# Optimization experiments

Measured on AMD Instinct MI355X. Metric: run time of the kernel, lower is better.

Reference implementation:

```python
import jax, jax.numpy as jnp
import numpy as np

N_NODES = 50000
N_HEDGES = 10000
NNZ_INC = 400000
NNZ_E = 80000
NNZ_V = 400000
VDIM = 128
EDIM = 128
OUT_VDIM = 128
OUT_EDIM = 128


def _spmm(rows, cols, vals, X, n_rows):
    # sparse COO [n_rows, n_cols] @ X  -> [n_rows, d]
    return jax.ops.segment_sum(vals[:, None] * X[cols], rows, num_segments=n_rows)


def setup_inputs() -> dict:
    key = jax.random.key(0)
    ks = jax.random.split(key, 20)
    inp = {
        "vfeat": jax.random.normal(ks[0], (N_NODES, VDIM), jnp.float32),
        "efeat": jax.random.normal(ks[1], (N_HEDGES, EDIM), jnp.float32),
        "invDV": jax.random.uniform(ks[2], (N_NODES,), jnp.float32),
        "invDE": jax.random.uniform(ks[3], (N_HEDGES,), jnp.float32),
        "inc_src": jax.random.randint(ks[4], (NNZ_INC,), 0, N_NODES, jnp.int32),
        "inc_dst": jax.random.randint(ks[5], (NNZ_INC,), 0, N_HEDGES, jnp.int32),
        "emat_rows": jax.random.randint(ks[6], (NNZ_E,), 0, N_HEDGES, jnp.int32),
        "emat_cols": jax.random.randint(ks[7], (NNZ_E,), 0, N_HEDGES, jnp.int32),
        "emat_vals": jax.random.normal(ks[8], (NNZ_E,), jnp.float32),
        "vmat_rows": jax.random.randint(ks[9], (NNZ_V,), 0, N_NODES, jnp.int32),
        "vmat_cols": jax.random.randint(ks[10], (NNZ_V,), 0, N_NODES, jnp.int32),
        "vmat_vals": jax.random.normal(ks[11], (NNZ_V,), jnp.float32),
        # parameters (torch Linear: y = x @ W.T + b)
        "Wv": jax.random.normal(ks[12], (OUT_VDIM, VDIM), jnp.float32) * 0.05,
        "We": jax.random.normal(ks[13], (OUT_EDIM, EDIM), jnp.float32) * 0.05,
        "psi1_W": jax.random.normal(ks[14], (VDIM, VDIM + EDIM), jnp.float32) * 0.05,
        "psi1_b": jnp.zeros((VDIM,), jnp.float32),
        "psi2_W": jax.random.normal(ks[15], (EDIM, OUT_VDIM + EDIM), jnp.float32) * 0.05,
        "psi2_b": jnp.zeros((EDIM,), jnp.float32),
    }
    return inp


def reference(vfeat, efeat, invDV, invDE, inc_src, inc_dst,
              emat_rows, emat_cols, emat_vals,
              vmat_rows, vmat_cols, vmat_vals,
              Wv, We, psi1_W, psi1_b, psi2_W, psi2_b):
    N = vfeat.shape[0]
    E = efeat.shape[0]
    # --- 'in' update_all with psi1: per-incidence concat -> linear -> *invDV[src] -> sum into hyperedge
    x = jnp.concatenate([vfeat[inc_src], efeat[inc_dst]], axis=1)  # [nnz, VDIM+EDIM]
    x = x @ psi1_W.T + psi1_b                                       # [nnz, VDIM]
    x = x * invDV[inc_src][:, None]
    A = jax.ops.segment_sum(x, inc_dst, num_segments=E)             # [E, VDIM]
    A = _spmm(emat_rows, emat_cols, emat_vals, A, E)
    _efeat = A + efeat
    # --- 'con' update_all: node gathers sum of incident hyperedge feats
    _vfeat = jax.ops.segment_sum(_efeat[inc_dst], inc_src, num_segments=N)
    vfeat_out = jax.nn.relu(_vfeat @ Wv.T)                           # [N, OUT_VDIM]
    # --- 'in' update_all with psi2 (dv = ones)
    x2 = jnp.concatenate([vfeat_out[inc_src], efeat[inc_dst]], axis=1)
    x2 = x2 @ psi2_W.T + psi2_b                                      # [nnz, EDIM]
    B = jax.ops.segment_sum(x2, inc_dst, num_segments=E) * invDE[:, None]
    # --- 'con' pass with efeat, then vMat spmm, then 'in' sum back to hyperedges
    _vfeat2 = jax.ops.segment_sum(efeat[inc_dst], inc_src, num_segments=N)
    _vfeat2 = _spmm(vmat_rows, vmat_cols, vmat_vals, _vfeat2, N)
    _efeat2 = jax.ops.segment_sum(_vfeat2[inc_src], inc_dst, num_segments=E)
    _efeat2 = _efeat2 + B
    efeat_out = jax.nn.relu(_efeat2 @ We.T)                          # [E, OUT_EDIM]
    return vfeat_out, efeat_out
```

## Files before the change

kernel.cpp:

```cpp
#include <hip/hip_runtime.h>

#define NN 50000
#define NE 10000
#define NNZ_INC 400000
#define NNZ_E 80000
#define NNZ_V 400000
#define D 128
#define KC 32

#define CAP_D 112
#define CAP_S 40
#define CAP_E 40
#define CAP_V 40

#define NE_SH (NE / 8)
#define NN_SH (NN / 8)

#define GN_ 782
#define GE_ 157
#define G_HINC ((NNZ_INC + 255) / 256)
#define G_HIST8 (8 * G_HINC)
#define G_EV ((NNZ_E + NNZ_V + 255) / 256)
#define G_CVTN 6250
#define G_CVTE 1250
#define G_NR16 (NN / 16)
#define G_ER16 (NE / 16)

typedef unsigned short u16;
typedef unsigned int u32;

__device__ __forceinline__ u16 f2bf(float x) {
    unsigned u = __float_as_uint(x);
    unsigned r = u + 0x7fffu + ((u >> 16) & 1u);
    return (u16)(r >> 16);
}
__device__ __forceinline__ float bf2f(u16 h) {
    return __uint_as_float(((unsigned)h) << 16);
}

__device__ __forceinline__ void acc8(uint4 u, float acc[8]) {
    acc[0] += __uint_as_float(u.x << 16);
    acc[1] += __uint_as_float(u.x & 0xffff0000u);
    acc[2] += __uint_as_float(u.y << 16);
    acc[3] += __uint_as_float(u.y & 0xffff0000u);
    acc[4] += __uint_as_float(u.z << 16);
    acc[5] += __uint_as_float(u.z & 0xffff0000u);
    acc[6] += __uint_as_float(u.w << 16);
    acc[7] += __uint_as_float(u.w & 0xffff0000u);
}
__device__ __forceinline__ void fma8(uint4 u, float v, float acc[8]) {
    acc[0] = fmaf(v, __uint_as_float(u.x << 16), acc[0]);
    acc[1] = fmaf(v, __uint_as_float(u.x & 0xffff0000u), acc[1]);
    acc[2] = fmaf(v, __uint_as_float(u.y << 16), acc[2]);
    acc[3] = fmaf(v, __uint_as_float(u.y & 0xffff0000u), acc[3]);
    acc[4] = fmaf(v, __uint_as_float(u.z << 16), acc[4]);
    acc[5] = fmaf(v, __uint_as_float(u.z & 0xffff0000u), acc[5]);
    acc[6] = fmaf(v, __uint_as_float(u.w << 16), acc[6]);
    acc[7] = fmaf(v, __uint_as_float(u.w & 0xffff0000u), acc[7]);
}
__device__ __forceinline__ uint4 pack_bf8(const float acc[8]) {
    uint4 o;
    o.x = (u32)f2bf(acc[0]) | ((u32)f2bf(acc[1]) << 16);
    o.y = (u32)f2bf(acc[2]) | ((u32)f2bf(acc[3]) << 16);
    o.z = (u32)f2bf(acc[4]) | ((u32)f2bf(acc[5]) << 16);
    o.w = (u32)f2bf(acc[6]) | ((u32)f2bf(acc[7]) << 16);
    return o;
}

__device__ __forceinline__ void gemm_acc(
    int bx, const float* __restrict__ X, const float* __restrict__ W, int ldw,
    int M, float acc[8][4])
{
    __shared__ float XsT[KC][68];
    __shared__ float Ws[KC][132];
    const int tid = threadIdx.x;
    const int tx = tid & 31, ty = tid >> 5;
    const int row0 = bx * 64;
    const int c0 = tx * 4;
    const int r0 = ty * 8;

#pragma unroll
    for (int r = 0; r < 8; ++r)
#pragma unroll
        for (int c = 0; c < 4; ++c) acc[r][c] = 0.f;

    for (int kc = 0; kc < D; kc += KC) {
        __syncthreads();
#pragma unroll
        for (int it = 0; it < 2; ++it) {
            int l = tid + it * 256;
            int r = l >> 3, k4 = l & 7;
            float4 v = make_float4(0.f, 0.f, 0.f, 0.f);
            int row = row0 + r;
            if (row < M) v = ((const float4*)(X + (size_t)row * D + kc))[k4];
            int k = k4 * 4;
            XsT[k + 0][r] = v.x; XsT[k + 1][r] = v.y;
            XsT[k + 2][r] = v.z; XsT[k + 3][r] = v.w;
        }
#pragma unroll
        for (int it = 0; it < 4; ++it) {
            int l = tid + it * 256;
            int o = l >> 3, k4 = l & 7;
            float4 w = ((const float4*)(W + (size_t)o * ldw + kc))[k4];
            int k = k4 * 4;
            Ws[k + 0][o] = w.x; Ws[k + 1][o] = w.y;
            Ws[k + 2][o] = w.z; Ws[k + 3][o] = w.w;
        }
        __syncthreads();
#pragma unroll
        for (int k = 0; k < KC; ++k) {
            const float4 a0 = *(const float4*)&XsT[k][r0];
            const float4 a1 = *(const float4*)&XsT[k][r0 + 4];
            const float4 b  = *(const float4*)&Ws[k][c0];
            float av[8] = {a0.x, a0.y, a0.z, a0.w, a1.x, a1.y, a1.z, a1.w};
            float bv[4] = {b.x, b.y, b.z, b.w};
#pragma unroll
            for (int r = 0; r < 8; ++r)
#pragma unroll
                for (int c = 0; c < 4; ++c)
                    acc[r][c] = fmaf(av[r], bv[c], acc[r][c]);
        }
    }
}

__device__ __forceinline__ void gemm_acc2(
    int bx, const float* __restrict__ X1, const float* __restrict__ X2,
    const float* __restrict__ rsf,
    const float* __restrict__ W, int M, float acc[8][4])
{
    __shared__ float XsT[KC][68];
    __shared__ float Ws[KC][132];
    const int tid = threadIdx.x;
    const int tx = tid & 31, ty = tid >> 5;
    const int row0 = bx * 64;
    const int c0 = tx * 4;
    const int r0 = ty * 8;

#pragma unroll
    for (int r = 0; r < 8; ++r)
#pragma unroll
        for (int c = 0; c < 4; ++c) acc[r][c] = 0.f;

    for (int kc = 0; kc < 2 * D; kc += KC) {
        __syncthreads();
        const bool second = (kc >= D);
        const float* Xp = second ? X2 : X1;
        const int kk = second ? kc - D : kc;
#pragma unroll
        for (int it = 0; it < 2; ++it) {
            int l = tid + it * 256;
            int r = l >> 3, k4 = l & 7;
            float4 v = make_float4(0.f, 0.f, 0.f, 0.f);
            int row = row0 + r;
            if (row < M) {
                v = ((const float4*)(Xp + (size_t)row * D + kk))[k4];
                if (second) {
                    float sc = rsf[row];
                    v.x *= sc; v.y *= sc; v.z *= sc; v.w *= sc;
                }
            }
            int k = k4 * 4;
            XsT[k + 0][r] = v.x; XsT[k + 1][r] = v.y;
            XsT[k + 2][r] = v.z; XsT[k + 3][r] = v.w;
        }
#pragma unroll
        for (int it = 0; it < 4; ++it) {
            int l = tid + it * 256;
            int o = l >> 3, k4 = l & 7;
            float4 w = ((const float4*)(W + (size_t)o * (2 * D) + kc))[k4];
            int k = k4 * 4;
            Ws[k + 0][o] = w.x; Ws[k + 1][o] = w.y;
            Ws[k + 2][o] = w.z; Ws[k + 3][o] = w.w;
        }
        __syncthreads();
#pragma unroll
        for (int k = 0; k < KC; ++k) {
            const float4 a0 = *(const float4*)&XsT[k][r0];
            const float4 a1 = *(const float4*)&XsT[k][r0 + 4];
            const float4 b  = *(const float4*)&Ws[k][c0];
            float av[8] = {a0.x, a0.y, a0.z, a0.w, a1.x, a1.y, a1.z, a1.w};
            float bv[4] = {b.x, b.y, b.z, b.w};
#pragma unroll
            for (int r = 0; r < 8; ++r)
#pragma unroll
                for (int c = 0; c < 4; ++c)
                    acc[r][c] = fmaf(av[r], bv[c], acc[r][c]);
        }
    }
}

__global__ __launch_bounds__(256) void mega0(
    const int* __restrict__ inc_src, const int* __restrict__ inc_dst,
    int* __restrict__ cnt_dst, int* __restrict__ cnt_src,
    u16* __restrict__ ell_d, u16* __restrict__ ell_s,
    const float* __restrict__ efeat, const float* __restrict__ vfeat,
    const float* __restrict__ invDV,
    u16* __restrict__ vfi_b, u16* __restrict__ efeat_b)
{
    int b = blockIdx.x;
    if (b < G_HIST8) {
        int shard = b & 7;
        int i = (b >> 3) * 256 + threadIdx.x;
        if (i < NNZ_INC) {
            int s = inc_src[i], d = inc_dst[i];
            if ((u32)(d - shard * NE_SH) < (u32)NE_SH) {
                int rd = atomicAdd(cnt_dst + d, 1);
                if (rd < CAP_D) ell_d[d * CAP_D + rd] = (u16)s;
            }
            if ((u32)(s - shard * NN_SH) < (u32)NN_SH) {
                int rs = atomicAdd(cnt_src + s, 1);
                if (rs < CAP_S) ell_s[s * CAP_S + rs] = (u16)d;
            }
        }
    } else if (b < G_HIST8 + G_CVTN) {
        int i = ((b - G_HIST8) * 256 + threadIdx.x) * 4;
        int row = i >> 7;
        float s = invDV[row];
        float4 v = *(const float4*)(vfeat + i);
        ushort4 u;
        u.x = f2bf(v.x * s); u.y = f2bf(v.y * s);
        u.z = f2bf(v.z * s); u.w = f2bf(v.w * s);
        *(ushort4*)(vfi_b + i) = u;
    } else {
        int i = ((b - G_HIST8 - G_CVTN) * 256 + threadIdx.x) * 4;
        float4 v = *(const float4*)(efeat + i);
        ushort4 u;
        u.x = f2bf(v.x); u.y = f2bf(v.y); u.z = f2bf(v.z); u.w = f2bf(v.w);
        *(ushort4*)(efeat_b + i) = u;
    }
}

__device__ __forceinline__ void segsum_bf_ell16(int rb,
    const int* __restrict__ cnt, int cap, const u16* __restrict__ ell,
    const u16* __restrict__ Tb, u16* __restrict__ Yb, int R)
{
    int r = rb * 16 + (threadIdx.x >> 4);
    int q = threadIdx.x & 15;
    if (r >= R) return;
    int m = min(cnt[r], cap);
    const u16* lst = ell + (size_t)r * cap;
    float acc[8] = {0.f, 0.f, 0.f, 0.f, 0.f, 0.f, 0.f, 0.f};
    int j = 0;
    for (; j + 3 < m; j += 4) {
        ushort4 ix = *(const ushort4*)(lst + j);
        uint4 u0 = *(const uint4*)(Tb + (size_t)ix.x * D + q * 8);
        uint4 u1 = *(const uint4*)(Tb + (size_t)ix.y * D + q * 8);
        uint4 u2 = *(const uint4*)(Tb + (size_t)ix.z * D + q * 8);
        uint4 u3 = *(const uint4*)(Tb + (size_t)ix.w * D + q * 8);
        acc8(u0, acc); acc8(u1, acc); acc8(u2, acc); acc8(u3, acc);
    }
    for (; j < m; ++j) {
        uint4 u0 = *(const uint4*)(Tb + (size_t)lst[j] * D + q * 8);
        acc8(u0, acc);
    }
    ((uint4*)(Yb + (size_t)r * D))[q] = pack_bf8(acc);
}

__device__ __forceinline__ void segsum_f_ell16(int rb,
    const int* __restrict__ cnt, int cap, const u16* __restrict__ ell,
    const u16* __restrict__ Tb, float* __restrict__ Y, int R)
{
    int r = rb * 16 + (threadIdx.x >> 4);
    int q = threadIdx.x & 15;
    if (r >= R) return;
    int m = min(cnt[r], cap);
    const u16* lst = ell + (size_t)r * cap;
    float acc[8] = {0.f, 0.f, 0.f, 0.f, 0.f, 0.f, 0.f, 0.f};
    int j = 0;
    for (; j + 7 < m; j += 8) {
        ushort4 ixa = *(const ushort4*)(lst + j);
        ushort4 ixb = *(const ushort4*)(lst + j + 4);
        uint4 u0 = *(const uint4*)(Tb + (size_t)ixa.x * D + q * 8);
        uint4 u1 = *(const uint4*)(Tb + (size_t)ixa.y * D + q * 8);
        uint4 u2 = *(const uint4*)(Tb + (size_t)ixa.z * D + q * 8);
        uint4 u3 = *(const uint4*)(Tb + (size_t)ixa.w * D + q * 8);
        uint4 u4 = *(const uint4*)(Tb + (size_t)ixb.x * D + q * 8);
        uint4 u5 = *(const uint4*)(Tb + (size_t)ixb.y * D + q * 8);
        uint4 u6 = *(const uint4*)(Tb + (size_t)ixb.z * D + q * 8);
        uint4 u7 = *(const uint4*)(Tb + (size_t)ixb.w * D + q * 8);
        acc8(u0, acc); acc8(u1, acc); acc8(u2, acc); acc8(u3, acc);
        acc8(u4, acc); acc8(u5, acc); acc8(u6, acc); acc8(u7, acc);
    }
    for (; j + 3 < m; j += 4) {
        ushort4 ix = *(const ushort4*)(lst + j);
        uint4 u0 = *(const uint4*)(Tb + (size_t)ix.x * D + q * 8);
        uint4 u1 = *(const uint4*)(Tb + (size_t)ix.y * D + q * 8);
        uint4 u2 = *(const uint4*)(Tb + (size_t)ix.z * D + q * 8);
        uint4 u3 = *(const uint4*)(Tb + (size_t)ix.w * D + q * 8);
        acc8(u0, acc); acc8(u1, acc); acc8(u2, acc); acc8(u3, acc);
    }
    for (; j < m; ++j) {
        uint4 u0 = *(const uint4*)(Tb + (size_t)lst[j] * D + q * 8);
        acc8(u0, acc);
    }
    float* yr = Y + (size_t)r * D;
    ((float4*)yr)[2 * q + 0] = make_float4(acc[0], acc[1], acc[2], acc[3]);
    ((float4*)yr)[2 * q + 1] = make_float4(acc[4], acc[5], acc[6], acc[7]);
}

__device__ __forceinline__ void spmm_bf_ell16(int rb,
    const int* __restrict__ cnt, int cap, const u32* __restrict__ ell,
    const u16* __restrict__ Xb, const float* __restrict__ addend,
    u16* __restrict__ Yb, int R)
{
    int r = rb * 16 + (threadIdx.x >> 4);
    int q = threadIdx.x & 15;
    if (r >= R) return;
    int m = min(cnt[r], cap);
    const u32* lst = ell + (size_t)r * cap;
    float acc[8];
    if (addend) {
        const float* ar = addend + (size_t)r * D;
        float4 lo = ((const float4*)ar)[2 * q + 0];
        float4 hi = ((const float4*)ar)[2 * q + 1];
        acc[0] = lo.x; acc[1] = lo.y; acc[2] = lo.z; acc[3] = lo.w;
        acc[4] = hi.x; acc[5] = hi.y; acc[6] = hi.z; acc[7] = hi.w;
    } else {
#pragma unroll
        for (int i = 0; i < 8; ++i) acc[i] = 0.f;
    }
    int j = 0;
    for (; j + 3 < m; j += 4) {
        uint4 e = *(const uint4*)(lst + j);
        uint4 x0 = *(const uint4*)(Xb + (size_t)(e.x >> 16) * D + q * 8);
        uint4 x1 = *(const uint4*)(Xb + (size_t)(e.y >> 16) * D + q * 8);
        uint4 x2 = *(const uint4*)(Xb + (size_t)(e.z >> 16) * D + q * 8);
        uint4 x3 = *(const uint4*)(Xb + (size_t)(e.w >> 16) * D + q * 8);
        fma8(x0, __uint_as_float(e.x << 16), acc);
        fma8(x1, __uint_as_float(e.y << 16), acc);
        fma8(x2, __uint_as_float(e.z << 16), acc);
        fma8(x3, __uint_as_float(e.w << 16), acc);
    }
    for (; j < m; ++j) {
        u32 e = lst[j];
        uint4 x = *(const uint4*)(Xb + (size_t)(e >> 16) * D + q * 8);
        fma8(x, __uint_as_float(e << 16), acc);
    }
    ((uint4*)(Yb + (size_t)r * D))[q] = pack_bf8(acc);
}

__global__ __launch_bounds__(256) void fusedA(
    const int* __restrict__ erows, const int* __restrict__ ecols,
    const float* __restrict__ evals, int* __restrict__ cnt_e, u32* __restrict__ ev_e,
    const int* __restrict__ vrows, const int* __restrict__ vcols,
    const float* __restrict__ vvals, int* __restrict__ cnt_v, u32* __restrict__ ev_v,
    const float* __restrict__ efeat,
    const float* __restrict__ psi2_W, const float* __restrict__ psi2_b, float* __restrict__ QeP,
    const int* __restrict__ cnt_dst, const u16* __restrict__ ell_d,
    const float* __restrict__ invDV, const u16* __restrict__ vfi_b,
    float* __restrict__ sva, float* __restrict__ wsum,
    const int* __restrict__ cnt_src, const u16* __restrict__ ell_s,
    const u16* __restrict__ efeat_b, u16* __restrict__ vf2_b)
{
    int b = blockIdx.x;
    if (b < G_EV) {
        int i = b * 256 + threadIdx.x;
        if (i < NNZ_E) {
            int r = erows[i];
            int re = atomicAdd(cnt_e + r, 1);
            if (re < CAP_E)
                ev_e[r * CAP_E + re] = ((u32)ecols[i] << 16) | (u32)f2bf(evals[i]);
        } else if (i < NNZ_E + NNZ_V) {
            int j = i - NNZ_E;
            int r = vrows[j];
            int rv = atomicAdd(cnt_v + r, 1);
            if (rv < CAP_V)
                ev_v[r * CAP_V + rv] = ((u32)vcols[j] << 16) | (u32)f2bf(vvals[j]);
        }
    } else if (b < G_EV + GE_) {
        int bx = b - G_EV;
        float acc[8][4];
        gemm_acc(bx, efeat, psi2_W + D, 2 * D, NE, acc);
        int tx = threadIdx.x & 31, ty = threadIdx.x >> 5;
        float4 b4 = ((const float4*)psi2_b)[tx];
#pragma unroll
        for (int r = 0; r < 8; ++r) {
            int row = bx * 64 + ty * 8 + r;
            if (row < NE) {
                float4 v = make_float4(acc[r][0] + b4.x, acc[r][1] + b4.y,
                                       acc[r][2] + b4.z, acc[r][3] + b4.w);
                ((float4*)(QeP + (size_t)row * D))[tx] = v;
            }
        }
    } else if (b < G_EV + GE_ + G_ER16) {
        int e = (b - G_EV - GE_) * 16 + (threadIdx.x >> 4);
        int q = threadIdx.x & 15;
        if (e >= NE) return;
        int m = min(cnt_dst[e], CAP_D);
        const u16* lst = ell_d + (size_t)e * CAP_D;
        float acc[8] = {0.f, 0.f, 0.f, 0.f, 0.f, 0.f, 0.f, 0.f};
        float ws = 0.f;
        int j = 0;
        for (; j + 3 < m; j += 4) {
            ushort4 ix = *(const ushort4*)(lst + j);
            uint4 u0 = *(const uint4*)(vfi_b + (size_t)ix.x * D + q * 8);
            uint4 u1 = *(const uint4*)(vfi_b + (size_t)ix.y * D + q * 8);
            uint4 u2 = *(const uint4*)(vfi_b + (size_t)ix.z * D + q * 8);
            uint4 u3 = *(const uint4*)(vfi_b + (size_t)ix.w * D + q * 8);
            ws += (invDV[ix.x] + invDV[ix.y]) + (invDV[ix.z] + invDV[ix.w]);
            acc8(u0, acc); acc8(u1, acc); acc8(u2, acc); acc8(u3, acc);
        }
        for (; j < m; ++j) {
            int s = lst[j];
            uint4 u0 = *(const uint4*)(vfi_b + (size_t)s * D + q * 8);
            ws += invDV[s];
            acc8(u0, acc);
        }
        float* yr = sva + (size_t)e * D;
        ((float4*)yr)[2 * q + 0] = make_float4(acc[0], acc[1], acc[2], acc[3]);
        ((float4*)yr)[2 * q + 1] = make_float4(acc[4], acc[5], acc[6], acc[7]);
        if (q == 0) wsum[e] = ws;
    } else {
        segsum_bf_ell16(b - G_EV - GE_ - G_ER16, cnt_src, CAP_S, ell_s, efeat_b, vf2_b, NN);
    }
}

__global__ __launch_bounds__(256) void fusedB2(
    const float* __restrict__ sva, const float* __restrict__ efeat,
    const float* __restrict__ wsum,
    const float* __restrict__ psi1_W, const float* __restrict__ psi1_b,
    u16* __restrict__ A_b,
    const int* __restrict__ cnt_v, const u32* __restrict__ ev_v,
    const u16* __restrict__ vf2_b, u16* __restrict__ vf2b_b)
{
    int b = blockIdx.x;
    if (b < GE_) {
        float acc[8][4];
        gemm_acc2(b, sva, efeat, wsum, psi1_W, NE, acc);
        int tx = threadIdx.x & 31, ty = threadIdx.x >> 5;
        float4 b4 = ((const float4*)psi1_b)[tx];
#pragma unroll
        for (int r = 0; r < 8; ++r) {
            int row = b * 64 + ty * 8 + r;
            if (row < NE) {
                float ws = wsum[row];
                ushort4 u;
                u.x = f2bf(fmaf(ws, b4.x, acc[r][0]));
                u.y = f2bf(fmaf(ws, b4.y, acc[r][1]));
                u.z = f2bf(fmaf(ws, b4.z, acc[r][2]));
                u.w = f2bf(fmaf(ws, b4.w, acc[r][3]));
                ((ushort4*)(A_b + (size_t)row * D))[tx] = u;
            }
        }
    } else {
        spmm_bf_ell16(b - GE_, cnt_v, CAP_V, ev_v, vf2_b, nullptr, vf2b_b, NN);
    }
}

__global__ __launch_bounds__(256) void fusedC2(
    const int* __restrict__ cnt_e, const u32* __restrict__ ev_e,
    const u16* __restrict__ A_b, const float* __restrict__ efeat, u16* __restrict__ A2_b,
    const int* __restrict__ cnt_dst, const u16* __restrict__ ell_d,
    const u16* __restrict__ vf2b_b, float* __restrict__ av)
{
    int b = blockIdx.x;
    if (b < G_ER16) spmm_bf_ell16(b, cnt_e, CAP_E, ev_e, A_b, efeat, A2_b, NE);
    else segsum_f_ell16(b - G_ER16, cnt_dst, CAP_D, ell_d, vf2b_b, av, NE);
}

__global__ __launch_bounds__(256) void fusedD2(
    const int* __restrict__ cnt_src, const u16* __restrict__ ell_s,
    const u16* __restrict__ A2_b, float* __restrict__ vf1)
{
    segsum_f_ell16(blockIdx.x, cnt_src, CAP_S, ell_s, A2_b, vf1, NN);
}

__global__ __launch_bounds__(256) void gemmC_k(
    const float* __restrict__ vf1, const float* __restrict__ Wv,
    float* __restrict__ out_v, u16* __restrict__ outv_b)
{
    float acc[8][4];
    gemm_acc(blockIdx.x, vf1, Wv, D, NN, acc);
    int tx = threadIdx.x & 31, ty = threadIdx.x >> 5;
#pragma unroll
    for (int r = 0; r < 8; ++r) {
        int row = blockIdx.x * 64 + ty * 8 + r;
        if (row < NN) {
            float4 v = make_float4(fmaxf(acc[r][0], 0.f), fmaxf(acc[r][1], 0.f),
                                   fmaxf(acc[r][2], 0.f), fmaxf(acc[r][3], 0.f));
            ((float4*)(out_v + (size_t)row * D))[tx] = v;
            ushort4 u;
            u.x = f2bf(v.x); u.y = f2bf(v.y); u.z = f2bf(v.z); u.w = f2bf(v.w);
            ((ushort4*)(outv_b + (size_t)row * D))[tx] = u;
        }
    }
}

__global__ __launch_bounds__(256) void gather_sv(
    const int* __restrict__ cnt_dst, const u16* __restrict__ ell_d,
    const u16* __restrict__ outv_b, float* __restrict__ sv)
{
    segsum_f_ell16(blockIdx.x, cnt_dst, CAP_D, ell_d, outv_b, sv, NE);
}

__global__ __launch_bounds__(256) void gemmBE_k(
    const float* __restrict__ sv, const float* __restrict__ psi2_W,
    const int* __restrict__ cnt_dst, const float* __restrict__ QeP,
    const float* __restrict__ invDE, const float* __restrict__ av,
    const float* __restrict__ We, float* __restrict__ out_e)
{
    __shared__ float T[D][68];
    float acc[8][4];
    gemm_acc(blockIdx.x, sv, psi2_W, 2 * D, NE, acc);
    const int tx = threadIdx.x & 31, ty = threadIdx.x >> 5;
    const int bx = blockIdx.x;
#pragma unroll
    for (int r = 0; r < 8; ++r) {
        int row = bx * 64 + ty * 8 + r;
        float deg = 0.f, ide = 0.f;
        float4 qe = make_float4(0.f, 0.f, 0.f, 0.f);
        float4 a  = make_float4(0.f, 0.f, 0.f, 0.f);
        if (row < NE) {
            deg = (float)cnt_dst[row];
            ide = invDE[row];
            qe = ((const float4*)(QeP + (size_t)row * D))[tx];
            a  = ((const float4*)(av  + (size_t)row * D))[tx];
        }
        int lr = ty * 8 + r;
        T[tx * 4 + 0][lr] = fmaf(deg, qe.x, acc[r][0]) * ide + a.x;
        T[tx * 4 + 1][lr] = fmaf(deg, qe.y, acc[r][1]) * ide + a.y;
        T[tx * 4 + 2][lr] = fmaf(deg, qe.z, acc[r][2]) * ide + a.z;
        T[tx * 4 + 3][lr] = fmaf(deg, qe.w, acc[r][3]) * ide + a.w;
    }
    __shared__ float Ws2[KC][132];
    float acc2[8][4];
#pragma unroll
    for (int r = 0; r < 8; ++r)
#pragma unroll
        for (int c = 0; c < 4; ++c) acc2[r][c] = 0.f;
    const int c0 = tx * 4, r0 = ty * 8;
    for (int kc = 0; kc < D; kc += KC) {
        __syncthreads();
#pragma unroll
        for (int it = 0; it < 4; ++it) {
            int l = threadIdx.x + it * 256;
            int o = l >> 3, k4 = l & 7;
            float4 w = ((const float4*)(We + (size_t)o * D + kc))[k4];
            int k = k4 * 4;
            Ws2[k + 0][o] = w.x; Ws2[k + 1][o] = w.y;
            Ws2[k + 2][o] = w.z; Ws2[k + 3][o] = w.w;
        }
        __syncthreads();
#pragma unroll
        for (int k = 0; k < KC; ++k) {
            const float4 a0 = *(const float4*)&T[kc + k][r0];
            const float4 a1 = *(const float4*)&T[kc + k][r0 + 4];
            const float4 bb = *(const float4*)&Ws2[k][c0];
            float avv[8] = {a0.x, a0.y, a0.z, a0.w, a1.x, a1.y, a1.z, a1.w};
            float bv[4] = {bb.x, bb.y, bb.z, bb.w};
#pragma unroll
            for (int r = 0; r < 8; ++r)
#pragma unroll
                for (int c = 0; c < 4; ++c)
                    acc2[r][c] = fmaf(avv[r], bv[c], acc2[r][c]);
        }
    }
#pragma unroll
    for (int r = 0; r < 8; ++r) {
        int row = bx * 64 + ty * 8 + r;
        if (row < NE) {
            float4 v = make_float4(fmaxf(acc2[r][0], 0.f), fmaxf(acc2[r][1], 0.f),
                                   fmaxf(acc2[r][2], 0.f), fmaxf(acc2[r][3], 0.f));
            ((float4*)(out_e + (size_t)row * D))[tx] = v;
        }
    }
}

extern "C" void kernel_launch(void* const* d_in, const int* in_sizes, int n_in,
                              void* d_out, int out_size, void* d_ws, size_t ws_size,
                              hipStream_t stream)
{
    (void)in_sizes; (void)n_in; (void)out_size; (void)ws_size;
    const float* vfeat     = (const float*)d_in[0];
    const float* efeat     = (const float*)d_in[1];
    const float* invDV     = (const float*)d_in[2];
    const float* invDE     = (const float*)d_in[3];
    const int*   inc_src   = (const int*)d_in[4];
    const int*   inc_dst   = (const int*)d_in[5];
    const int*   emat_rows = (const int*)d_in[6];
    const int*   emat_cols = (const int*)d_in[7];
    const float* emat_vals = (const float*)d_in[8];
    const int*   vmat_rows = (const int*)d_in[9];
    const int*   vmat_cols = (const int*)d_in[10];
    const float* vmat_vals = (const float*)d_in[11];
    const float* Wv        = (const float*)d_in[12];
    const float* We        = (const float*)d_in[13];
    const float* psi1_W    = (const float*)d_in[14];
    const float* psi1_b    = (const float*)d_in[15];
    const float* psi2_W    = (const float*)d_in[16];
    const float* psi2_b    = (const float*)d_in[17];

    const size_t ND = (size_t)NN * D;
    const size_t ED = (size_t)NE * D;

    char* p = (char*)d_ws;
    auto alloc = [&](size_t bytes) {
        size_t a = (size_t)p; a = (a + 255) & ~(size_t)255;
        p = (char*)a; void* r = (void*)p; p += bytes; return r;
    };
    float* QeP   = (float*)alloc(ED * 4);
    float* vf1   = (float*)alloc(ND * 4);
    float* av    = (float*)alloc(ED * 4);
    float* svbuf = (float*)alloc(ED * 4);
    float* wsum  = (float*)alloc((size_t)NE * 4);
    u16* vfi_b   = (u16*)alloc(ND * 2);
    u16* outv_b  = (u16*)alloc(ND * 2);
    u16* vf2_b   = (u16*)alloc(ND * 2);
    u16* vf2b_b  = (u16*)alloc(ND * 2);
    u16* efeat_b = (u16*)alloc(ED * 2);
    u16* A_b     = (u16*)alloc(ED * 2);
    u16* A2_b    = (u16*)alloc(ED * 2);
    int* cnt_dst = (int*)alloc((size_t)(2 * NE + 2 * NN) * 4);
    int* cnt_src = cnt_dst + NE;
    int* cnt_e   = cnt_src + NN;
    int* cnt_v   = cnt_e + NE;
    u16* ell_d   = (u16*)alloc((size_t)NE * CAP_D * 2);
    u16* ell_s   = (u16*)alloc((size_t)NN * CAP_S * 2);
    u32* ev_e    = (u32*)alloc((size_t)NE * CAP_E * 4);
    u32* ev_v    = (u32*)alloc((size_t)NN * CAP_V * 4);

    float* out_v = (float*)d_out;
    float* out_e = out_v + ND;

    dim3 b256(256);

    hipMemsetAsync(cnt_dst, 0, (size_t)(2 * NE + 2 * NN) * sizeof(int), stream);
    mega0<<<G_HIST8 + G_CVTN + G_CVTE, b256, 0, stream>>>(
        inc_src, inc_dst, cnt_dst, cnt_src, ell_d, ell_s,
        efeat, vfeat, invDV, vfi_b, efeat_b);
    fusedA<<<G_EV + GE_ + G_ER16 + G_NR16, b256, 0, stream>>>(
        emat_rows, emat_cols, emat_vals, cnt_e, ev_e,
        vmat_rows, vmat_cols, vmat_vals, cnt_v, ev_v,
        efeat, psi2_W, psi2_b, QeP,
        cnt_dst, ell_d, invDV, vfi_b, svbuf, wsum,
        cnt_src, ell_s, efeat_b, vf2_b);
    fusedB2<<<GE_ + G_NR16, b256, 0, stream>>>(
        svbuf, efeat, wsum, psi1_W, psi1_b, A_b,
        cnt_v, ev_v, vf2_b, vf2b_b);
    fusedC2<<<G_ER16 + G_ER16, b256, 0, stream>>>(
        cnt_e, ev_e, A_b, efeat, A2_b,
        cnt_dst, ell_d, vf2b_b, av);
    fusedD2<<<G_NR16, b256, 0, stream>>>(cnt_src, ell_s, A2_b, vf1);
    gemmC_k<<<GN_, b256, 0, stream>>>(vf1, Wv, out_v, outv_b);
    gather_sv<<<G_ER16, b256, 0, stream>>>(cnt_dst, ell_d, outv_b, svbuf);
    gemmBE_k<<<GE_, b256, 0, stream>>>(svbuf, psi2_W, cnt_dst, QeP, invDE, av, We, out_e);
}
```

Before: 362.5 us.

## Apply Wv on hyperedge side before node gather, add ELL sorting, fold COO build into mega0

Uses linearity to move the Wv projection from the 50000-row node GEMM to the 10000-row hyperedge side. It applies Wv to efeat and to the psi1 output, chained inside fusedB2, so the node pass becomes a gather-sum plus ReLU. This removes the separate node GEMM kernel and the fp32 vf1 intermediate. The emat/vmat COO-to-ELL build moves into the first mega kernel. A new insertion-sort kernel orders each ELL row's indices to improve gather locality, at the cost of an extra launch and serial per-thread sorting.

```diff
diff --git a/kernel.cpp b/kernel.cpp
--- a/kernel.cpp
+++ b/kernel.cpp
@@ -16,15 +16,16 @@
 #define NE_SH (NE / 8)
 #define NN_SH (NN / 8)
 
-#define GN_ 782
 #define GE_ 157
 #define G_HINC ((NNZ_INC + 255) / 256)
 #define G_HIST8 (8 * G_HINC)
-#define G_EV ((NNZ_E + NNZ_V + 255) / 256)
+#define G_EVB ((NNZ_E + NNZ_V + 255) / 256)
 #define G_CVTN 6250
 #define G_CVTE 1250
 #define G_NR16 (NN / 16)
 #define G_ER16 (NE / 16)
+#define G_SORT_D 40
+#define G_SORT_V 196
 
 typedef unsigned short u16;
 typedef unsigned int u32;
@@ -123,76 +124,14 @@
     }
 }
 
-__device__ __forceinline__ void gemm_acc2(
-    int bx, const float* __restrict__ X1, const float* __restrict__ X2,
-    const float* __restrict__ rsf,
-    const float* __restrict__ W, int M, float acc[8][4])
-{
-    __shared__ float XsT[KC][68];
-    __shared__ float Ws[KC][132];
-    const int tid = threadIdx.x;
-    const int tx = tid & 31, ty = tid >> 5;
-    const int row0 = bx * 64;
-    const int c0 = tx * 4;
-    const int r0 = ty * 8;
-
-#pragma unroll
-    for (int r = 0; r < 8; ++r)
-#pragma unroll
-        for (int c = 0; c < 4; ++c) acc[r][c] = 0.f;
-
-    for (int kc = 0; kc < 2 * D; kc += KC) {
-        __syncthreads();
-        const bool second = (kc >= D);
-        const float* Xp = second ? X2 : X1;
-        const int kk = second ? kc - D : kc;
-#pragma unroll
-        for (int it = 0; it < 2; ++it) {
-            int l = tid + it * 256;
-            int r = l >> 3, k4 = l & 7;
-            float4 v = make_float4(0.f, 0.f, 0.f, 0.f);
-            int row = row0 + r;
-            if (row < M) {
-                v = ((const float4*)(Xp + (size_t)row * D + kk))[k4];
-                if (second) {
-                    float sc = rsf[row];
-                    v.x *= sc; v.y *= sc; v.z *= sc; v.w *= sc;
-                }
-            }
-            int k = k4 * 4;
-            XsT[k + 0][r] = v.x; XsT[k + 1][r] = v.y;
-            XsT[k + 2][r] = v.z; XsT[k + 3][r] = v.w;
-        }
-#pragma unroll
-        for (int it = 0; it < 4; ++it) {
-            int l = tid + it * 256;
-            int o = l >> 3, k4 = l & 7;
-            float4 w = ((const float4*)(W + (size_t)o * (2 * D) + kc))[k4];
-            int k = k4 * 4;
-            Ws[k + 0][o] = w.x; Ws[k + 1][o] = w.y;
-            Ws[k + 2][o] = w.z; Ws[k + 3][o] = w.w;
-        }
-        __syncthreads();
-#pragma unroll
-        for (int k = 0; k < KC; ++k) {
-            const float4 a0 = *(const float4*)&XsT[k][r0];
-            const float4 a1 = *(const float4*)&XsT[k][r0 + 4];
-            const float4 b  = *(const float4*)&Ws[k][c0];
-            float av[8] = {a0.x, a0.y, a0.z, a0.w, a1.x, a1.y, a1.z, a1.w};
-            float bv[4] = {b.x, b.y, b.z, b.w};
-#pragma unroll
-            for (int r = 0; r < 8; ++r)
-#pragma unroll
-                for (int c = 0; c < 4; ++c)
-                    acc[r][c] = fmaf(av[r], bv[c], acc[r][c]);
-        }
-    }
-}
-
 __global__ __launch_bounds__(256) void mega0(
     const int* __restrict__ inc_src, const int* __restrict__ inc_dst,
     int* __restrict__ cnt_dst, int* __restrict__ cnt_src,
     u16* __restrict__ ell_d, u16* __restrict__ ell_s,
+    const int* __restrict__ erows, const int* __restrict__ ecols,
+    const float* __restrict__ evals, int* __restrict__ cnt_e, u32* __restrict__ ev_e,
+    const int* __restrict__ vrows, const int* __restrict__ vcols,
+    const float* __restrict__ vvals, int* __restrict__ cnt_v, u32* __restrict__ ev_v,
     const float* __restrict__ efeat, const float* __restrict__ vfeat,
     const float* __restrict__ invDV,
     u16* __restrict__ vfi_b, u16* __restrict__ efeat_b)
@@ -212,8 +151,22 @@
                 if (rs < CAP_S) ell_s[s * CAP_S + rs] = (u16)d;
             }
         }
-    } else if (b < G_HIST8 + G_CVTN) {
-        int i = ((b - G_HIST8) * 256 + threadIdx.x) * 4;
+    } else if (b < G_HIST8 + G_EVB) {
+        int i = (b - G_HIST8) * 256 + threadIdx.x;
+        if (i < NNZ_E) {
+            int r = erows[i];
+            int re = atomicAdd(cnt_e + r, 1);
+            if (re < CAP_E)
+                ev_e[r * CAP_E + re] = ((u32)ecols[i] << 16) | (u32)f2bf(evals[i]);
+        } else if (i < NNZ_E + NNZ_V) {
+            int j = i - NNZ_E;
+            int r = vrows[j];
+            int rv = atomicAdd(cnt_v + r, 1);
+            if (rv < CAP_V)
+                ev_v[r * CAP_V + rv] = ((u32)vcols[j] << 16) | (u32)f2bf(vvals[j]);
+        }
+    } else if (b < G_HIST8 + G_EVB + G_CVTN) {
+        int i = ((b - G_HIST8 - G_EVB) * 256 + threadIdx.x) * 4;
         int row = i >> 7;
         float s = invDV[row];
         float4 v = *(const float4*)(vfeat + i);
@@ -222,11 +175,41 @@
         u.z = f2bf(v.z * s); u.w = f2bf(v.w * s);
         *(ushort4*)(vfi_b + i) = u;
     } else {
-        int i = ((b - G_HIST8 - G_CVTN) * 256 + threadIdx.x) * 4;
+        int i = ((b - G_HIST8 - G_EVB - G_CVTN) * 256 + threadIdx.x) * 4;
         float4 v = *(const float4*)(efeat + i);
         ushort4 u;
         u.x = f2bf(v.x); u.y = f2bf(v.y); u.z = f2bf(v.z); u.w = f2bf(v.w);
         *(ushort4*)(efeat_b + i) = u;
+    }
+}
+
+__global__ __launch_bounds__(256) void sortk(
+    const int* __restrict__ cnt_dst, u16* __restrict__ ell_d,
+    const int* __restrict__ cnt_v, u32* __restrict__ ev_v)
+{
+    int b = blockIdx.x;
+    if (b < G_SORT_D) {
+        int r = b * 256 + threadIdx.x;
+        if (r >= NE) return;
+        int m = min(cnt_dst[r], CAP_D);
+        u16* a = ell_d + (size_t)r * CAP_D;
+        for (int i = 1; i < m; ++i) {
+            u16 key = a[i];
+            int j = i - 1;
+            while (j >= 0 && a[j] > key) { a[j + 1] = a[j]; --j; }
+            a[j + 1] = key;
+        }
+    } else {
+        int r = (b - G_SORT_D) * 256 + threadIdx.x;
+        if (r >= NN) return;
+        int m = min(cnt_v[r], CAP_V);
+        u32* a = ev_v + (size_t)r * CAP_V;
+        for (int i = 1; i < m; ++i) {
+            u32 key = a[i];
+            int j = i - 1;
+            while (j >= 0 && a[j] > key) { a[j + 1] = a[j]; --j; }
+            a[j + 1] = key;
+        }
     }
 }
 
@@ -340,12 +323,9 @@
 }
 
 __global__ __launch_bounds__(256) void fusedA(
-    const int* __restrict__ erows, const int* __restrict__ ecols,
-    const float* __restrict__ evals, int* __restrict__ cnt_e, u32* __restrict__ ev_e,
-    const int* __restrict__ vrows, const int* __restrict__ vcols,
-    const float* __restrict__ vvals, int* __restrict__ cnt_v, u32* __restrict__ ev_v,
     const float* __restrict__ efeat,
     const float* __restrict__ psi2_W, const float* __restrict__ psi2_b, float* __restrict__ QeP,
+    const float* __restrict__ Wv, float* __restrict__ efP,
     const int* __restrict__ cnt_dst, const u16* __restrict__ ell_d,
     const float* __restrict__ invDV, const u16* __restrict__ vfi_b,
     float* __restrict__ sva, float* __restrict__ wsum,
@@ -353,37 +333,8 @@
     const u16* __restrict__ efeat_b, u16* __restrict__ vf2_b)
 {
     int b = blockIdx.x;
-    if (b < G_EV) {
-        int i = b * 256 + threadIdx.x;
-        if (i < NNZ_E) {
-            int r = erows[i];
-            int re = atomicAdd(cnt_e + r, 1);
-            if (re < CAP_E)
-                ev_e[r * CAP_E + re] = ((u32)ecols[i] << 16) | (u32)f2bf(evals[i]);
-        } else if (i < NNZ_E + NNZ_V) {
-            int j = i - NNZ_E;
-            int r = vrows[j];
-            int rv = atomicAdd(cnt_v + r, 1);
-            if (rv < CAP_V)
-                ev_v[r * CAP_V + rv] = ((u32)vcols[j] << 16) | (u32)f2bf(vvals[j]);
-        }
-    } else if (b < G_EV + GE_) {
-        int bx = b - G_EV;
-        float acc[8][4];
-        gemm_acc(bx, efeat, psi2_W + D, 2 * D, NE, acc);
-        int tx = threadIdx.x & 31, ty = threadIdx.x >> 5;
-        float4 b4 = ((const float4*)psi2_b)[tx];
-#pragma unroll
-        for (int r = 0; r < 8; ++r) {
-            int row = bx * 64 + ty * 8 + r;
-            if (row < NE) {
-                float4 v = make_float4(acc[r][0] + b4.x, acc[r][1] + b4.y,
-                                       acc[r][2] + b4.z, acc[r][3] + b4.w);
-                ((float4*)(QeP + (size_t)row * D))[tx] = v;
-            }
-        }
-    } else if (b < G_EV + GE_ + G_ER16) {
-        int e = (b - G_EV - GE_) * 16 + (threadIdx.x >> 4);
+    if (b < G_ER16) {
+        int e = b * 16 + (threadIdx.x >> 4);
         int q = threadIdx.x & 15;
         if (e >= NE) return;
         int m = min(cnt_dst[e], CAP_D);
@@ -410,8 +361,36 @@
         ((float4*)yr)[2 * q + 0] = make_float4(acc[0], acc[1], acc[2], acc[3]);
         ((float4*)yr)[2 * q + 1] = make_float4(acc[4], acc[5], acc[6], acc[7]);
         if (q == 0) wsum[e] = ws;
+    } else if (b < G_ER16 + GE_) {
+        int bx = b - G_ER16;
+        float acc[8][4];
+        gemm_acc(bx, efeat, psi2_W + D, 2 * D, NE, acc);
+        int tx = threadIdx.x & 31, ty = threadIdx.x >> 5;
+        float4 b4 = ((const float4*)psi2_b)[tx];
+#pragma unroll
+        for (int r = 0; r < 8; ++r) {
+            int row = bx * 64 + ty * 8 + r;
+            if (row < NE) {
+                float4 v = make_float4(acc[r][0] + b4.x, acc[r][1] + b4.y,
+                                       acc[r][2] + b4.z, acc[r][3] + b4.w);
+                ((float4*)(QeP + (size_t)row * D))[tx] = v;
+            }
+        }
+    } else if (b < G_ER16 + 2 * GE_) {
+        int bx = b - G_ER16 - GE_;
+        float acc[8][4];
+        gemm_acc(bx, efeat, Wv, D, NE, acc);
+        int tx = threadIdx.x & 31, ty = threadIdx.x >> 5;
+#pragma unroll
+        for (int r = 0; r < 8; ++r) {
+            int row = bx * 64 + ty * 8 + r;
+            if (row < NE) {
+                float4 v = make_float4(acc[r][0], acc[r][1], acc[r][2], acc[r][3]);
+                ((float4*)(efP + (size_t)row * D))[tx] = v;
+            }
+        }
     } else {
-        segsum_bf_ell16(b - G_EV - GE_ - G_ER16, cnt_src, CAP_S, ell_s, efeat_b, vf2_b, NN);
+        segsum_bf_ell16(b - G_ER16 - 2 * GE_, cnt_src, CAP_S, ell_s, efeat_b, vf2_b, NN);
     }
 }
 
@@ -419,71 +398,176 @@
     const float* __restrict__ sva, const float* __restrict__ efeat,
     const float* __restrict__ wsum,
     const float* __restrict__ psi1_W, const float* __restrict__ psi1_b,
-    u16* __restrict__ A_b,
+    const float* __restrict__ Wv, u16* __restrict__ AP_b,
     const int* __restrict__ cnt_v, const u32* __restrict__ ev_v,
     const u16* __restrict__ vf2_b, u16* __restrict__ vf2b_b)
 {
     int b = blockIdx.x;
-    if (b < GE_) {
-        float acc[8][4];
-        gemm_acc2(b, sva, efeat, wsum, psi1_W, NE, acc);
-        int tx = threadIdx.x & 31, ty = threadIdx.x >> 5;
-        float4 b4 = ((const float4*)psi1_b)[tx];
-#pragma unroll
-        for (int r = 0; r < 8; ++r) {
-            int row = b * 64 + ty * 8 + r;
+    if (b < G_NR16) {
+        spmm_bf_ell16(b, cnt_v, CAP_V, ev_v, vf2_b, nullptr, vf2b_b, NN);
+        return;
+    }
+    __shared__ float XsT[KC][68];
+    __shared__ float Ws[KC][132];
+    const int bx = b - G_NR16;
+    const int tid = threadIdx.x;
+    const int tx = tid & 31, ty = tid >> 5;
+    const int row0 = bx * 64;
+    const int c0 = tx * 4;
+    const int r0 = ty * 8;
+    float acc[8][4];
+#pragma unroll
+    for (int r = 0; r < 8; ++r)
+#pragma unroll
+        for (int c = 0; c < 4; ++c) acc[r][c] = 0.f;
+
+    for (int kc = 0; kc < 2 * D; kc += KC) {
+        __syncthreads();
+        const bool second = (kc >= D);
+        const float* Xp = second ? efeat : sva;
+        const int kk = second ? kc - D : kc;
+#pragma unroll
+        for (int it = 0; it < 2; ++it) {
+            int l = tid + it * 256;
+            int r = l >> 3, k4 = l & 7;
+            float4 v = make_float4(0.f, 0.f, 0.f, 0.f);
+            int row = row0 + r;
             if (row < NE) {
-                float ws = wsum[row];
-                ushort4 u;
-                u.x = f2bf(fmaf(ws, b4.x, acc[r][0]));
-                u.y = f2bf(fmaf(ws, b4.y, acc[r][1]));
-                u.z = f2bf(fmaf(ws, b4.z, acc[r][2]));
-                u.w = f2bf(fmaf(ws, b4.w, acc[r][3]));
-                ((ushort4*)(A_b + (size_t)row * D))[tx] = u;
+                v = ((const float4*)(Xp + (size_t)row * D + kk))[k4];
+                if (second) {
+                    float sc = wsum[row];
+                    v.x *= sc; v.y *= sc; v.z *= sc; v.w *= sc;
+                }
             }
-        }
-    } else {
-        spmm_bf_ell16(b - GE_, cnt_v, CAP_V, ev_v, vf2_b, nullptr, vf2b_b, NN);
+            int k = k4 * 4;
+            XsT[k + 0][r] = v.x; XsT[k + 1][r] = v.y;
+            XsT[k + 2][r] = v.z; XsT[k + 3][r] = v.w;
+        }
+#pragma unroll
+        for (int it = 0; it < 4; ++it) {
+            int l = tid + it * 256;
+            int o = l >> 3, k4 = l & 7;
+            float4 w = ((const float4*)(psi1_W + (size_t)o * (2 * D) + kc))[k4];
+            int k = k4 * 4;
+            Ws[k + 0][o] = w.x; Ws[k + 1][o] = w.y;
+            Ws[k + 2][o] = w.z; Ws[k + 3][o] = w.w;
+        }
+        __syncthreads();
+#pragma unroll
+        for (int k = 0; k < KC; ++k) {
+            const float4 a0 = *(const float4*)&XsT[k][r0];
+            const float4 a1 = *(const float4*)&XsT[k][r0 + 4];
+            const float4 bb = *(const float4*)&Ws[k][c0];
+            float av[8] = {a0.x, a0.y, a0.z, a0.w, a1.x, a1.y, a1.z, a1.w};
+            float bv[4] = {bb.x, bb.y, bb.z, bb.w};
+#pragma unroll
+            for (int r = 0; r < 8; ++r)
+#pragma unroll
+                for (int c = 0; c < 4; ++c)
+                    acc[r][c] = fmaf(av[r], bv[c], acc[r][c]);
+        }
+    }
+    float4 b4 = ((const float4*)psi1_b)[tx];
+    float wsv[8];
+#pragma unroll
+    for (int r = 0; r < 8; ++r) {
+        int row = row0 + r0 + r;
+        wsv[r] = (row < NE) ? wsum[row] : 0.f;
+    }
+    float accP[8][4];
+#pragma unroll
+    for (int r = 0; r < 8; ++r)
+#pragma unroll
+        for (int c = 0; c < 4; ++c) accP[r][c] = 0.f;
+
+    for (int kc = 0; kc < D; kc += KC) {
+        __syncthreads();
+        if ((u32)(tx - (kc >> 2)) < 8u) {
+            int kk0 = tx * 4 - kc;
+#pragma unroll
+            for (int r = 0; r < 8; ++r) {
+                XsT[kk0 + 0][r0 + r] = fmaf(wsv[r], b4.x, acc[r][0]);
+                XsT[kk0 + 1][r0 + r] = fmaf(wsv[r], b4.y, acc[r][1]);
+                XsT[kk0 + 2][r0 + r] = fmaf(wsv[r], b4.z, acc[r][2]);
+                XsT[kk0 + 3][r0 + r] = fmaf(wsv[r], b4.w, acc[r][3]);
+            }
+        }
+#pragma unroll
+        for (int it = 0; it < 4; ++it) {
+            int l = tid + it * 256;
+            int o = l >> 3, k4 = l & 7;
+            float4 w = ((const float4*)(Wv + (size_t)o * D + kc))[k4];
+            int k = k4 * 4;
+            Ws[k + 0][o] = w.x; Ws[k + 1][o] = w.y;
+            Ws[k + 2][o] = w.z; Ws[k + 3][o] = w.w;
+        }
+        __syncthreads();
+#pragma unroll
+        for (int k = 0; k < KC; ++k) {
+            const float4 a0 = *(const float4*)&XsT[k][r0];
+            const float4 a1 = *(const float4*)&XsT[k][r0 + 4];
+            const float4 bb = *(const float4*)&Ws[k][c0];
+            float av[8] = {a0.x, a0.y, a0.z, a0.w, a1.x, a1.y, a1.z, a1.w};
+            float bv[4] = {bb.x, bb.y, bb.z, bb.w};
+#pragma unroll
+            for (int r = 0; r < 8; ++r)
+#pragma unroll
+                for (int c = 0; c < 4; ++c)
+                    accP[r][c] = fmaf(av[r], bv[c], accP[r][c]);
+        }
+    }
+#pragma unroll
+    for (int r = 0; r < 8; ++r) {
+        int row = row0 + r0 + r;
+        if (row < NE) {
+            ushort4 u;
+            u.x = f2bf(accP[r][0]); u.y = f2bf(accP[r][1]);
+            u.z = f2bf(accP[r][2]); u.w = f2bf(accP[r][3]);
+            ((ushort4*)(AP_b + (size_t)row * D))[tx] = u;
+        }
     }
 }
 
 __global__ __launch_bounds__(256) void fusedC2(
+    const int* __restrict__ cnt_dst, const u16* __restrict__ ell_d,
+    const u16* __restrict__ vf2b_b, float* __restrict__ av,
     const int* __restrict__ cnt_e, const u32* __restrict__ ev_e,
-    const u16* __restrict__ A_b, const float* __restrict__ efeat, u16* __restrict__ A2_b,
-    const int* __restrict__ cnt_dst, const u16* __restrict__ ell_d,
-    const u16* __restrict__ vf2b_b, float* __restrict__ av)
+    const u16* __restrict__ AP_b, const float* __restrict__ efP, u16* __restrict__ A2P_b)
 {
     int b = blockIdx.x;
-    if (b < G_ER16) spmm_bf_ell16(b, cnt_e, CAP_E, ev_e, A_b, efeat, A2_b, NE);
-    else segsum_f_ell16(b - G_ER16, cnt_dst, CAP_D, ell_d, vf2b_b, av, NE);
-}
-
-__global__ __launch_bounds__(256) void fusedD2(
+    if (b < G_ER16) segsum_f_ell16(b, cnt_dst, CAP_D, ell_d, vf2b_b, av, NE);
+    else spmm_bf_ell16(b - G_ER16, cnt_e, CAP_E, ev_e, AP_b, efP, A2P_b, NE);
+}
+
+__global__ __launch_bounds__(256) void outv_k(
     const int* __restrict__ cnt_src, const u16* __restrict__ ell_s,
-    const u16* __restrict__ A2_b, float* __restrict__ vf1)
-{
-    segsum_f_ell16(blockIdx.x, cnt_src, CAP_S, ell_s, A2_b, vf1, NN);
-}
-
-__global__ __launch_bounds__(256) void gemmC_k(
-    const float* __restrict__ vf1, const float* __restrict__ Wv,
-    float* __restrict__ out_v, u16* __restrict__ outv_b)
-{
-    float acc[8][4];
-    gemm_acc(blockIdx.x, vf1, Wv, D, NN, acc);
-    int tx = threadIdx.x & 31, ty = threadIdx.x >> 5;
-#pragma unroll
-    for (int r = 0; r < 8; ++r) {
-        int row = blockIdx.x * 64 + ty * 8 + r;
-        if (row < NN) {
-            float4 v = make_float4(fmaxf(acc[r][0], 0.f), fmaxf(acc[r][1], 0.f),
-                                   fmaxf(acc[r][2], 0.f), fmaxf(acc[r][3], 0.f));
-            ((float4*)(out_v + (size_t)row * D))[tx] = v;
-            ushort4 u;
-            u.x = f2bf(v.x); u.y = f2bf(v.y); u.z = f2bf(v.z); u.w = f2bf(v.w);
-            ((ushort4*)(outv_b + (size_t)row * D))[tx] = u;
-        }
-    }
+    const u16* __restrict__ A2P_b, float* __restrict__ out_v, u16* __restrict__ outv_b)
+{
+    int r = blockIdx.x * 16 + (threadIdx.x >> 4);
+    int q = threadIdx.x & 15;
+    if (r >= NN) return;
+    int m = min(cnt_src[r], CAP_S);
+    const u16* lst = ell_s + (size_t)r * CAP_S;
+    float acc[8] = {0.f, 0.f, 0.f, 0.f, 0.f, 0.f, 0.f, 0.f};
+    int j = 0;
+    for (; j + 3 < m; j += 4) {
+        ushort4 ix = *(const ushort4*)(lst + j);
+        uint4 u0 = *(const uint4*)(A2P_b + (size_t)ix.x * D + q * 8);
+        uint4 u1 = *(const uint4*)(A2P_b + (size_t)ix.y * D + q * 8);
+        uint4 u2 = *(const uint4*)(A2P_b + (size_t)ix.z * D + q * 8);
+        uint4 u3 = *(const uint4*)(A2P_b + (size_t)ix.w * D + q * 8);
+        acc8(u0, acc); acc8(u1, acc); acc8(u2, acc); acc8(u3, acc);
+    }
+    for (; j < m; ++j) {
+        uint4 u0 = *(const uint4*)(A2P_b + (size_t)lst[j] * D + q * 8);
+        acc8(u0, acc);
+    }
+#pragma unroll
+    for (int i = 0; i < 8; ++i) acc[i] = fmaxf(acc[i], 0.f);
+    float* yr = out_v + (size_t)r * D;
+    ((float4*)yr)[2 * q + 0] = make_float4(acc[0], acc[1], acc[2], acc[3]);
+    ((float4*)yr)[2 * q + 1] = make_float4(acc[4], acc[5], acc[6], acc[7]);
+    ((uint4*)(outv_b + (size_t)r * D))[q] = pack_bf8(acc);
 }
 
 __global__ __launch_bounds__(256) void gather_sv(
@@ -599,7 +683,7 @@
         p = (char*)a; void* r = (void*)p; p += bytes; return r;
     };
     float* QeP   = (float*)alloc(ED * 4);
-    float* vf1   = (float*)alloc(ND * 4);
+    float* efP   = (float*)alloc(ED * 4);
     float* av    = (float*)alloc(ED * 4);
     float* svbuf = (float*)alloc(ED * 4);
     float* wsum  = (float*)alloc((size_t)NE * 4);
@@ -608,8 +692,8 @@
     u16* vf2_b   = (u16*)alloc(ND * 2);
     u16* vf2b_b  = (u16*)alloc(ND * 2);
     u16* efeat_b = (u16*)alloc(ED * 2);
-    u16* A_b     = (u16*)alloc(ED * 2);
-    u16* A2_b    = (u16*)alloc(ED * 2);
+    u16* AP_b    = (u16*)alloc(ED * 2);
+    u16* A2P_b   = (u16*)alloc(ED * 2);
     int* cnt_dst = (int*)alloc((size_t)(2 * NE + 2 * NN) * 4);
     int* cnt_src = cnt_dst + NE;
     int* cnt_e   = cnt_src + NN;
@@ -625,23 +709,23 @@
     dim3 b256(256);
 
     hipMemsetAsync(cnt_dst, 0, (size_t)(2 * NE + 2 * NN) * sizeof(int), stream);
-    mega0<<<G_HIST8 + G_CVTN + G_CVTE, b256, 0, stream>>>(
+    mega0<<<G_HIST8 + G_EVB + G_CVTN + G_CVTE, b256, 0, stream>>>(
         inc_src, inc_dst, cnt_dst, cnt_src, ell_d, ell_s,
-        efeat, vfeat, invDV, vfi_b, efeat_b);
-    fusedA<<<G_EV + GE_ + G_ER16 + G_NR16, b256, 0, stream>>>(
         emat_rows, emat_cols, emat_vals, cnt_e, ev_e,
         vmat_rows, vmat_cols, vmat_vals, cnt_v, ev_v,
-        efeat, psi2_W, psi2_b, QeP,
+        efeat, vfeat, invDV, vfi_b, efeat_b);
+    sortk<<<G_SORT_D + G_SORT_V, b256, 0, stream>>>(cnt_dst, ell_d, cnt_v, ev_v);
+    fusedA<<<G_ER16 + 2 * GE_ + G_NR16, b256, 0, stream>>>(
+        efeat, psi2_W, psi2_b, QeP, Wv, efP,
         cnt_dst, ell_d, invDV, vfi_b, svbuf, wsum,
         cnt_src, ell_s, efeat_b, vf2_b);
-    fusedB2<<<GE_ + G_NR16, b256, 0, stream>>>(
-        svbuf, efeat, wsum, psi1_W, psi1_b, A_b,
+    fusedB2<<<G_NR16 + GE_, b256, 0, stream>>>(
+        svbuf, efeat, wsum, psi1_W, psi1_b, Wv, AP_b,
         cnt_v, ev_v, vf2_b, vf2b_b);
     fusedC2<<<G_ER16 + G_ER16, b256, 0, stream>>>(
-        cnt_e, ev_e, A_b, efeat, A2_b,
-        cnt_dst, ell_d, vf2b_b, av);
-    fusedD2<<<G_NR16, b256, 0, stream>>>(cnt_src, ell_s, A2_b, vf1);
-    gemmC_k<<<GN_, b256, 0, stream>>>(vf1, Wv, out_v, outv_b);
+        cnt_dst, ell_d, vf2b_b, av,
+        cnt_e, ev_e, AP_b, efP, A2P_b);
+    outv_k<<<G_NR16, b256, 0, stream>>>(cnt_src, ell_s, A2P_b, out_v, outv_b);
     gather_sv<<<G_ER16, b256, 0, stream>>>(cnt_dst, ell_d, outv_b, svbuf);
     gemmBE_k<<<GE_, b256, 0, stream>>>(svbuf, psi2_W, cnt_dst, QeP, invDE, av, We, out_e);
 }
```

After: 708.7 us. +95.5%, slower.
